# Performance work log

Measured on AMD Instinct MI355X. Metric: run time of the kernel, lower is better.

The kernel has to match this reference:

```python
import jax, jax.numpy as jnp
import numpy as np

B, N, E_PER = 64, 1024, 32768
IN_DIM, HID, K = 128, 128, 64
EPS = 1e-15


def setup_inputs() -> dict:
    key = jax.random.key(0)
    ks = jax.random.split(key, 16)
    x = jax.random.normal(ks[0], (B * N, IN_DIM), jnp.float32)
    off = (jnp.arange(B, dtype=jnp.int32) * N)[:, None]
    src = (jax.random.randint(ks[1], (B, E_PER), 0, N, dtype=jnp.int32) + off).reshape(-1)
    dst = (jax.random.randint(ks[2], (B, E_PER), 0, N, dtype=jnp.int32) + off).reshape(-1)
    edge_index = jnp.stack([src, dst])
    batch = jnp.repeat(jnp.arange(B, dtype=jnp.int32), N)

    def lin(k, i, o):
        return (jax.random.normal(k, (i, o), jnp.float32) / np.sqrt(i)).astype(jnp.float32)

    params = dict(
        W1l=lin(ks[3], IN_DIM, HID), b1l=jnp.zeros((HID,), jnp.float32), W1r=lin(ks[4], IN_DIM, HID),
        W2l=lin(ks[5], HID, K), b2l=jnp.zeros((K,), jnp.float32), W2r=lin(ks[6], HID, K),
        Wm=lin(ks[7], K, K), bm=jnp.zeros((K,), jnp.float32),
        Wrel=lin(ks[8], HID, HID), Wroot=lin(ks[9], HID, HID), broot=jnp.zeros((HID,), jnp.float32),
        Wc1=lin(ks[10], HID * K, HID), bc1=jnp.zeros((HID,), jnp.float32),
        Wc2=lin(ks[11], HID, 1), bc2=jnp.zeros((1,), jnp.float32),
    )
    return dict(x=x, edge_index=edge_index, batch=batch, num_graphs=B, nodes_per_graph=N, **params)


def _sage(x, src, dst, Wl, bl, Wr, n):
    # PyG SAGEConv: lin_l(mean_{j in N(i)} x_j) + lin_r(x_i); lin_r has no bias.
    agg = jax.ops.segment_sum(x[src], dst, num_segments=n)
    deg = jax.ops.segment_sum(jnp.ones((src.shape[0],), x.dtype), dst, num_segments=n)
    agg = agg / jnp.maximum(deg, 1.0)[:, None]
    return agg @ Wl + bl + x @ Wr


def reference(x, edge_index, batch, num_graphs, nodes_per_graph,
              W1l, b1l, W1r, W2l, b2l, W2r, Wm, bm,
              Wrel, Wroot, broot, Wc1, bc1, Wc2, bc2):
    Bn, Nn = num_graphs, nodes_per_graph
    n_total = Bn * Nn
    src, dst = edge_index[0], edge_index[1]

    z = jax.nn.leaky_relu(_sage(x, src, dst, W1l, b1l, W1r, n_total), 0.01)
    s = jax.nn.leaky_relu(_sage(z, src, dst, W2l, b2l, W2r, n_total), 0.01)
    s = s @ Wm + bm

    # to_dense_batch (equal-size graphs -> mask all True) and to_dense_adj
    z = z.reshape(Bn, Nn, -1)                      # [B, N, HID]
    s = s.reshape(Bn, Nn, -1)                      # [B, N, K]
    a = jnp.zeros((Bn, Nn, Nn), x.dtype).at[src // Nn, src % Nn, dst % Nn].add(1.0)

    # dense_diff_pool
    s = jax.nn.softmax(s, axis=-1)
    pooled = jnp.einsum('bnk,bnf->bkf', s, z)      # [B, K, HID]
    adj_p = jnp.einsum('bnk,bnm,bml->bkl', s, a, s)  # [B, K, K]
    link_loss = jnp.sqrt(jnp.sum((a - jnp.einsum('bnk,bmk->bnm', s, s)) ** 2)) / a.size
    ent_loss = jnp.mean(jnp.sum(-s * jnp.log(s + EPS), axis=-1))

    # DenseSAGEConv: lin_rel(adj@x / deg) + lin_root(x)
    agg = jnp.matmul(adj_p, pooled) / jnp.maximum(adj_p.sum(-1, keepdims=True), 1.0)
    h = jax.nn.leaky_relu(agg @ Wrel + pooled @ Wroot + broot, 0.01)

    h = h.reshape(Bn, -1)                          # [B, K*HID]
    logits = (jax.nn.leaky_relu(h @ Wc1 + bc1, 0.01) @ Wc2 + bc2).squeeze(-1)
    return logits, link_loss + ent_loss
```

## Files before the change

kernel.cpp:

```cpp
#include <hip/hip_runtime.h>
#include <math.h>

#define BATCH 64
#define NPG 1024
#define NT (BATCH*NPG)
#define EPER 32768
#define ETOT (BATCH*EPER)

typedef __attribute__((ext_vector_type(4))) float f32x4;
typedef __attribute__((ext_vector_type(8))) short s16x8;

__device__ __forceinline__ float lky(float x){ return x > 0.f ? x : 0.01f*x; }
__device__ __forceinline__ unsigned short f2bf(float f){
    unsigned u = __float_as_uint(f);
    u = u + 0x7FFFu + ((u >> 16) & 1u);
    return (unsigned short)(u >> 16);
}
__device__ __forceinline__ float bf2f_lo(unsigned v){ return __uint_as_float(v << 16); }
__device__ __forceinline__ float bf2f_hi(unsigned v){ return __uint_as_float(v & 0xFFFF0000u); }

__global__ void k_castx(const float* __restrict__ in, unsigned short* __restrict__ out, int n4){
    int i = blockIdx.x*256 + threadIdx.x;
    if (i < n4){
        float4 v = ((const float4*)in)[i];
        ushort4 o = { f2bf(v.x), f2bf(v.y), f2bf(v.z), f2bf(v.w) };
        ((ushort4*)out)[i] = o;
    }
}

__global__ void k_wprep(const float* __restrict__ W1l, const float* __restrict__ W1r,
                        const float* __restrict__ W2l, const float* __restrict__ W2r,
                        unsigned short* __restrict__ wt){
    int i = blockIdx.x*256 + threadIdx.x;
    if (i < 16384){ int k = i >> 7, n = i & 127; wt[n*128 + k] = f2bf(W1l[i]); }
    else if (i < 32768){ int j = i - 16384; int k = j >> 7, n = j & 127; wt[16384 + n*128 + k] = f2bf(W1r[j]); }
    else if (i < 40960){ int j = i - 32768; int k = j >> 6, n = j & 63; wt[32768 + n*128 + k] = f2bf(W2l[j]); }
    else if (i < 49152){ int j = i - 40960; int k = j >> 6, n = j & 63; wt[40960 + n*128 + k] = f2bf(W2r[j]); }
}

__global__ void __launch_bounds__(1024) k_a2lds(const int* __restrict__ src, const int* __restrict__ dst,
                                                unsigned* __restrict__ acc_out){
    __shared__ unsigned nib[32768];
    __shared__ unsigned red[16];
    int b = blockIdx.x, pass = blockIdx.y, tid = threadIdx.x;
    for (int i = tid; i < 32768; i += 1024) nib[i] = 0;
    __syncthreads();
    int base = b*EPER;
    for (int i = tid; i < EPER; i += 1024){
        unsigned key = (((unsigned)src[base+i] & 1023u) << 10) | ((unsigned)dst[base+i] & 1023u);
        if ((int)(key >> 18) == pass)
            atomicAdd(&nib[(key & 0x3FFFFu) >> 3], 1u << ((key & 7u)*4u));
    }
    __syncthreads();
    unsigned local = 0;
    for (int i = tid; i < 32768; i += 1024){
        unsigned w = nib[i];
        if (w){
            #pragma unroll
            for (int q = 0; q < 8; q++){ unsigned c = (w >> (4*q)) & 15u; local += c*c; }
        }
    }
    for (int o = 32; o; o >>= 1) local += __shfl_xor(local, o);
    if ((tid & 63) == 0) red[tid >> 6] = local;
    __syncthreads();
    if (tid == 0){
        unsigned s = 0;
        for (int q = 0; q < 16; q++) s += red[q];
        atomicAdd(acc_out, s);
    }
}

__global__ void __launch_bounds__(1024) k_csr(const int* __restrict__ src, const int* __restrict__ dst,
                                              int* __restrict__ ipd, int* __restrict__ ips,
                                              unsigned short* __restrict__ lst_d,
                                              unsigned short* __restrict__ lst_s){
    __shared__ unsigned eds[EPER];
    __shared__ int cnt[1024];
    __shared__ int buf[1024];
    int g = blockIdx.x, which = blockIdx.y, tid = threadIdx.x;
    cnt[tid] = 0;
    __syncthreads();
    int base = g*EPER;
    for (int i = tid; i < EPER; i += 1024){
        unsigned s = (unsigned)src[base+i] & 1023u;
        unsigned d = (unsigned)dst[base+i] & 1023u;
        eds[i] = (s << 10) | d;
        atomicAdd(&cnt[which ? s : d], 1);
    }
    __syncthreads();
    int v = cnt[tid];
    int x = v;
    buf[tid] = x; __syncthreads();
    for (int off = 1; off < 1024; off <<= 1){
        int t = (tid >= off) ? buf[tid - off] : 0;
        __syncthreads();
        x += t; buf[tid] = x; __syncthreads();
    }
    int excl = x - v;
    int* ip = which ? ips : ipd;
    ip[g*1024 + tid] = base + excl;
    if (g == 0 && tid == 0) ip[NT] = ETOT;
    cnt[tid] = excl;
    __syncthreads();
    unsigned short* lst = which ? lst_s : lst_d;
    for (int i = tid; i < EPER; i += 1024){
        unsigned key = eds[i];
        unsigned d = key & 1023u, s = key >> 10;
        unsigned idx = which ? s : d;
        unsigned val = which ? d : s;
        int p = atomicAdd(&cnt[idx], 1);
        lst[base + p] = (unsigned short)val;
    }
}

template<int MODE, int TD>
__global__ void __launch_bounds__(1024) k_aggl(
        const unsigned short* __restrict__ X, const int* __restrict__ indptr,
        const unsigned short* __restrict__ lst,
        const unsigned short* __restrict__ R, const float* __restrict__ bias,
        unsigned short* __restrict__ out){
    __shared__ uint2 tab[1024*17];
    int bid = blockIdx.x;
    int xcd = bid & 7, j = bid >> 3;
    int gi = j >> 2, part = j & 3;
    int graph = xcd + 8*gi;
    int half, nbase_loc, nchunks;
    if (TD == 128){ half = part >> 1; nbase_loc = (part & 1)*512; nchunks = 8; }
    else          { half = 0;         nbase_loc = part*256;       nchunks = 4; }
    int foff = half*64;
    int tid = threadIdx.x;
    int gb = graph*NPG;
    for (int i = tid; i < 16384; i += 1024){
        int row = i >> 4, q = i & 15;
        tab[row*17 + q] = *(const uint2*)&X[(size_t)(gb+row)*TD + foff + q*4];
    }
    __syncthreads();
    int g = tid & 15;
    for (int c = 0; c < nchunks; c++){
        int node = gb + nbase_loc + c*64 + (tid >> 4);
        int st = indptr[node], en = indptr[node+1];
        float a0 = 0.f, a1 = 0.f, a2 = 0.f, a3 = 0.f;
        int e = st;
        for (; e + 4 <= en; e += 4){
            int r0 = lst[e+0], r1 = lst[e+1], r2 = lst[e+2], r3 = lst[e+3];
            uint2 v0 = tab[r0*17 + g];
            uint2 v1 = tab[r1*17 + g];
            uint2 v2 = tab[r2*17 + g];
            uint2 v3 = tab[r3*17 + g];
            a0 += bf2f_lo(v0.x) + bf2f_lo(v1.x) + bf2f_lo(v2.x) + bf2f_lo(v3.x);
            a1 += bf2f_hi(v0.x) + bf2f_hi(v1.x) + bf2f_hi(v2.x) + bf2f_hi(v3.x);
            a2 += bf2f_lo(v0.y) + bf2f_lo(v1.y) + bf2f_lo(v2.y) + bf2f_lo(v3.y);
            a3 += bf2f_hi(v0.y) + bf2f_hi(v1.y) + bf2f_hi(v2.y) + bf2f_hi(v3.y);
        }
        for (; e < en; e++){
            uint2 v = tab[lst[e]*17 + g];
            a0 += bf2f_lo(v.x); a1 += bf2f_hi(v.x);
            a2 += bf2f_lo(v.y); a3 += bf2f_hi(v.y);
        }
        if (MODE >= 1){
            int dg = en - st;
            float inv = 1.f/(float)(dg > 1 ? dg : 1);
            a0 *= inv; a1 *= inv; a2 *= inv; a3 *= inv;
        }
        if (MODE == 2){
            uint2 r = *(const uint2*)&R[(size_t)node*TD + foff + 4*g];
            a0 = lky(a0 + bf2f_lo(r.x) + bias[foff + 4*g + 0]);
            a1 = lky(a1 + bf2f_hi(r.x) + bias[foff + 4*g + 1]);
            a2 = lky(a2 + bf2f_lo(r.y) + bias[foff + 4*g + 2]);
            a3 = lky(a3 + bf2f_hi(r.y) + bias[foff + 4*g + 3]);
        }
        uint2 pk;
        pk.x = (unsigned)f2bf(a0) | ((unsigned)f2bf(a1) << 16);
        pk.y = (unsigned)f2bf(a2) | ((unsigned)f2bf(a3) << 16);
        *(uint2*)&out[(size_t)node*TD + foff + 4*g] = pk;
    }
}

template<int N>
__global__ void __launch_bounds__(512) k_mfma2b(
        const unsigned short* __restrict__ Ah, const unsigned short* __restrict__ Wt1,
        const unsigned short* __restrict__ Wt2, unsigned short* __restrict__ C1,
        unsigned short* __restrict__ C2){
    __shared__ unsigned short ldsB[2*N*128];
    int tid = threadIdx.x;
    for (int i = tid; i < N*64; i += 512){
        int n = i >> 6, kk = i & 63;
        int swz = (n*256 + 4*kk) ^ ((n & 7) << 4);
        *(unsigned*)((char*)ldsB + swz)         = ((const unsigned*)Wt1)[i];
        *(unsigned*)((char*)ldsB + N*256 + swz) = ((const unsigned*)Wt2)[i];
    }
    __syncthreads();
    int wave = tid >> 6, l = tid & 63;
    int lr = l & 15, lg = l >> 4;
    constexpr int NF = N/16;
    int arow = blockIdx.x*128 + wave*16 + lr;
    f32x4 acc1[NF], acc2[NF];
    f32x4 zv = {0.f, 0.f, 0.f, 0.f};
    #pragma unroll
    for (int nf = 0; nf < NF; nf++){ acc1[nf] = zv; acc2[nf] = zv; }
    #pragma unroll
    for (int ks = 0; ks < 4; ks++){
        s16x8 af = *(const s16x8*)(Ah + (size_t)arow*128 + ks*32 + lg*8);
        #pragma unroll
        for (int nf = 0; nf < NF; nf++){
            int n = nf*16 + lr;
            int swz = (n*256 + ks*64 + lg*16) ^ ((n & 7) << 4);
            s16x8 b1 = *(const s16x8*)((const char*)ldsB + swz);
            s16x8 b2 = *(const s16x8*)((const char*)ldsB + N*256 + swz);
            acc1[nf] = __builtin_amdgcn_mfma_f32_16x16x32_bf16(af, b1, acc1[nf], 0, 0, 0);
            acc2[nf] = __builtin_amdgcn_mfma_f32_16x16x32_bf16(af, b2, acc2[nf], 0, 0, 0);
        }
    }
    int orow = blockIdx.x*128 + wave*16 + lg*4;
    #pragma unroll
    for (int nf = 0; nf < NF; nf++){
        int c = nf*16 + lr;
        #pragma unroll
        for (int j = 0; j < 4; j++){
            size_t idx = (size_t)(orow + j)*N + c;
            C1[idx] = f2bf(acc1[nf][j]);
            C2[idx] = f2bf(acc2[nf][j]);
        }
    }
}

__global__ void __launch_bounds__(256) k_gemm(
        const float* __restrict__ A1, const float* __restrict__ A2,
        const float* __restrict__ W1, const float* __restrict__ W2,
        const float* __restrict__ bias, void* __restrict__ C,
        int M, int Nn, int Kd, int dual, int act, int obf){
    __shared__ float sA1[16*68], sB1[16*68], sA2[16*68], sB2[16*68];
    int tid = threadIdx.x;
    int m0 = blockIdx.x*64, n0 = blockIdx.y*64;
    int tx = tid & 15, ty = tid >> 4;
    int lr = tid >> 2, lk = (tid & 3)*4;
    int wk = tid >> 4, wn = (tid & 15)*4;
    float acc[4][4] = {};
    for (int k0 = 0; k0 < Kd; k0 += 16){
        float4 a1 = *(const float4*)&A1[(size_t)(m0+lr)*Kd + k0 + lk];
        float4 w1 = *(const float4*)&W1[(size_t)(k0+wk)*Nn + n0 + wn];
        sA1[(lk+0)*68+lr] = a1.x; sA1[(lk+1)*68+lr] = a1.y;
        sA1[(lk+2)*68+lr] = a1.z; sA1[(lk+3)*68+lr] = a1.w;
        *(float4*)&sB1[wk*68+wn] = w1;
        if (dual){
            float4 a2 = *(const float4*)&A2[(size_t)(m0+lr)*Kd + k0 + lk];
            float4 w2 = *(const float4*)&W2[(size_t)(k0+wk)*Nn + n0 + wn];
            sA2[(lk+0)*68+lr] = a2.x; sA2[(lk+1)*68+lr] = a2.y;
            sA2[(lk+2)*68+lr] = a2.z; sA2[(lk+3)*68+lr] = a2.w;
            *(float4*)&sB2[wk*68+wn] = w2;
        }
        __syncthreads();
        #pragma unroll
        for (int kk = 0; kk < 16; kk++){
            float4 av = *(const float4*)&sA1[kk*68 + ty*4];
            float4 bv = *(const float4*)&sB1[kk*68 + tx*4];
            float a[4] = {av.x, av.y, av.z, av.w};
            float b[4] = {bv.x, bv.y, bv.z, bv.w};
            #pragma unroll
            for (int i = 0; i < 4; i++)
                #pragma unroll
                for (int j = 0; j < 4; j++) acc[i][j] += a[i]*b[j];
            if (dual){
                float4 av2 = *(const float4*)&sA2[kk*68 + ty*4];
                float4 bv2 = *(const float4*)&sB2[kk*68 + tx*4];
                float a2[4] = {av2.x, av2.y, av2.z, av2.w};
                float b2[4] = {bv2.x, bv2.y, bv2.z, bv2.w};
                #pragma unroll
                for (int i = 0; i < 4; i++)
                    #pragma unroll
                    for (int j = 0; j < 4; j++) acc[i][j] += a2[i]*b2[j];
            }
        }
        __syncthreads();
    }
    float bb[4] = {0.f, 0.f, 0.f, 0.f};
    if (bias){
        #pragma unroll
        for (int j = 0; j < 4; j++) bb[j] = bias[n0 + tx*4 + j];
    }
    #pragma unroll
    for (int i = 0; i < 4; i++){
        float v0 = acc[i][0]+bb[0], v1 = acc[i][1]+bb[1], v2 = acc[i][2]+bb[2], v3 = acc[i][3]+bb[3];
        if (act){ v0 = lky(v0); v1 = lky(v1); v2 = lky(v2); v3 = lky(v3); }
        size_t idx = (size_t)(m0 + ty*4 + i)*Nn + n0 + tx*4;
        if (obf){
            ushort4 o = { f2bf(v0), f2bf(v1), f2bf(v2), f2bf(v3) };
            *(ushort4*)&((unsigned short*)C)[idx] = o;
        } else {
            float4 o = { v0, v1, v2, v3 };
            *(float4*)&((float*)C)[idx] = o;
        }
    }
}

__global__ void __launch_bounds__(256) k_gemm_wm(
        const unsigned short* __restrict__ agg2h, const unsigned short* __restrict__ r2h,
        const float* __restrict__ b2l, const float* __restrict__ Wm,
        const float* __restrict__ bm,
        unsigned short* __restrict__ Sh, float* __restrict__ ent_acc){
    __shared__ float sA[16*68], sB[16*68];
    __shared__ float red[256];
    int tid = threadIdx.x;
    int m0 = blockIdx.x*64;
    int tx = tid & 15, ty = tid >> 4;
    int lr = tid >> 2, lk = (tid & 3)*4;
    int wk = tid >> 4, wn = (tid & 15)*4;
    float acc[4][4] = {};
    for (int k0 = 0; k0 < 64; k0 += 16){
        uint2 a = *(const uint2*)&agg2h[(size_t)(m0+lr)*64 + k0 + lk];
        uint2 r = *(const uint2*)&r2h[(size_t)(m0+lr)*64 + k0 + lk];
        sA[(lk+0)*68+lr] = lky(bf2f_lo(a.x) + bf2f_lo(r.x) + b2l[k0+lk+0]);
        sA[(lk+1)*68+lr] = lky(bf2f_hi(a.x) + bf2f_hi(r.x) + b2l[k0+lk+1]);
        sA[(lk+2)*68+lr] = lky(bf2f_lo(a.y) + bf2f_lo(r.y) + b2l[k0+lk+2]);
        sA[(lk+3)*68+lr] = lky(bf2f_hi(a.y) + bf2f_hi(r.y) + b2l[k0+lk+3]);
        *(float4*)&sB[wk*68+wn] = *(const float4*)&Wm[(size_t)(k0+wk)*64 + wn];
        __syncthreads();
        #pragma unroll
        for (int kk = 0; kk < 16; kk++){
            float4 av = *(const float4*)&sA[kk*68 + ty*4];
            float4 bv = *(const float4*)&sB[kk*68 + tx*4];
            float a4[4] = {av.x, av.y, av.z, av.w};
            float b4[4] = {bv.x, bv.y, bv.z, bv.w};
            #pragma unroll
            for (int i = 0; i < 4; i++)
                #pragma unroll
                for (int j = 0; j < 4; j++) acc[i][j] += a4[i]*b4[j];
        }
        __syncthreads();
    }
    float bb[4];
    #pragma unroll
    for (int j = 0; j < 4; j++) bb[j] = bm[tx*4 + j];
    float ent_local = 0.f;
    #pragma unroll
    for (int i = 0; i < 4; i++){
        float v[4];
        #pragma unroll
        for (int j = 0; j < 4; j++) v[j] = acc[i][j] + bb[j];
        float m = fmaxf(fmaxf(v[0], v[1]), fmaxf(v[2], v[3]));
        for (int o = 1; o < 16; o <<= 1) m = fmaxf(m, __shfl_xor(m, o));
        float e[4];
        float sm = 0.f;
        #pragma unroll
        for (int j = 0; j < 4; j++){ e[j] = __expf(v[j] - m); sm += e[j]; }
        for (int o = 1; o < 16; o <<= 1) sm += __shfl_xor(sm, o);
        float inv = 1.f/sm;
        float p[4];
        float w = 0.f;
        #pragma unroll
        for (int j = 0; j < 4; j++){
            p[j] = e[j]*inv;
            w += -p[j]*__logf(p[j] + 1e-15f);
        }
        for (int o = 1; o < 16; o <<= 1) w += __shfl_xor(w, o);
        if (tx == 0) ent_local += w;
        size_t idx = (size_t)(m0 + ty*4 + i)*64 + tx*4;
        ushort4 oh = { f2bf(p[0]), f2bf(p[1]), f2bf(p[2]), f2bf(p[3]) };
        *(ushort4*)&Sh[idx] = oh;
    }
    red[tid] = ent_local; __syncthreads();
    for (int o = 128; o; o >>= 1){ if (tid < o) red[tid] += red[tid+o]; __syncthreads(); }
    if (tid == 0) atomicAdd(ent_acc, red[0]);
}

__global__ void __launch_bounds__(1024) k_spmm(
        const unsigned short* __restrict__ Sh, const unsigned short* __restrict__ Zh,
        const unsigned short* __restrict__ Th,
        float* __restrict__ P, float* __restrict__ AP, float* __restrict__ GR,
        float* __restrict__ crossp, float* __restrict__ normgp){
    __shared__ unsigned short At[64*72];
    __shared__ unsigned short Bt[256*72];
    __shared__ float rtr[16], rsq[16];
    int b = blockIdx.x, tid = threadIdx.x;
    int w = tid >> 6, l = tid & 63;
    int lr = l & 15, lg = l >> 4;
    int mt = w & 3, ng = w >> 2;
    f32x4 acc[4];
    f32x4 zv = {0.f, 0.f, 0.f, 0.f};
    #pragma unroll
    for (int q = 0; q < 4; q++) acc[q] = zv;
    int gb = b*NPG;
    int sa_n = tid & 63, sa_c = (tid >> 6)*4;
    int sb_k = tid & 63, sb_g = tid >> 6;
    for (int n0 = 0; n0 < NPG; n0 += 64){
        ushort4 sv = *(const ushort4*)&Sh[(size_t)(gb+n0+sa_n)*64 + sa_c];
        At[(sa_c+0)*72 + sa_n] = sv.x;
        At[(sa_c+1)*72 + sa_n] = sv.y;
        At[(sa_c+2)*72 + sa_n] = sv.z;
        At[(sa_c+3)*72 + sa_n] = sv.w;
        {
            int R = gb + n0 + sb_k;
            const unsigned short* srcp;
            if (sb_g < 8)       srcp = &Zh[(size_t)R*128 + sb_g*16];
            else if (sb_g < 12) srcp = &Th[(size_t)R*64 + (sb_g-8)*16];
            else                srcp = &Sh[(size_t)R*64 + (sb_g-12)*16];
            ushort4 a0 = *(const ushort4*)(srcp);
            ushort4 a1 = *(const ushort4*)(srcp+4);
            ushort4 a2 = *(const ushort4*)(srcp+8);
            ushort4 a3 = *(const ushort4*)(srcp+12);
            int cb = sb_g*16;
            Bt[(cb+ 0)*72+sb_k]=a0.x; Bt[(cb+ 1)*72+sb_k]=a0.y; Bt[(cb+ 2)*72+sb_k]=a0.z; Bt[(cb+ 3)*72+sb_k]=a0.w;
            Bt[(cb+ 4)*72+sb_k]=a1.x; Bt[(cb+ 5)*72+sb_k]=a1.y; Bt[(cb+ 6)*72+sb_k]=a1.z; Bt[(cb+ 7)*72+sb_k]=a1.w;
            Bt[(cb+ 8)*72+sb_k]=a2.x; Bt[(cb+ 9)*72+sb_k]=a2.y; Bt[(cb+10)*72+sb_k]=a2.z; Bt[(cb+11)*72+sb_k]=a2.w;
            Bt[(cb+12)*72+sb_k]=a3.x; Bt[(cb+13)*72+sb_k]=a3.y; Bt[(cb+14)*72+sb_k]=a3.z; Bt[(cb+15)*72+sb_k]=a3.w;
        }
        __syncthreads();
        #pragma unroll
        for (int ks = 0; ks < 2; ks++){
            s16x8 af = *(const s16x8*)&At[(mt*16+lr)*72 + ks*32 + lg*8];
            #pragma unroll
            for (int q = 0; q < 4; q++){
                s16x8 bf = *(const s16x8*)&Bt[((ng*4+q)*16+lr)*72 + ks*32 + lg*8];
                acc[q] = __builtin_amdgcn_mfma_f32_16x16x32_bf16(af, bf, acc[q], 0, 0, 0);
            }
        }
        __syncthreads();
    }
    float tr = 0.f, sq = 0.f;
    #pragma unroll
    for (int q = 0; q < 4; q++){
        int col = (ng*4+q)*16 + lr;
        #pragma unroll
        for (int j = 0; j < 4; j++){
            int m = mt*16 + lg*4 + j;
            float v = acc[q][j];
            if (col < 128){
                P[((size_t)b*64+m)*128 + col] = v;
            } else if (col < 192){
                AP[((size_t)b*64+m)*64 + (col-128)] = v;
                if (col-128 == m) tr += v;
            } else {
                GR[((size_t)b*64+m)*64 + (col-192)] = v;
                sq += v*v;
            }
        }
    }
    for (int o = 32; o; o >>= 1){ tr += __shfl_xor(tr, o); sq += __shfl_xor(sq, o); }
    if (l == 0){ rtr[w] = tr; rsq[w] = sq; }
    __syncthreads();
    if (tid == 0){
        float str = 0.f, ssq = 0.f;
        for (int i = 0; i < 16; i++){ str += rtr[i]; ssq += rsq[i]; }
        atomicAdd(crossp, str);
        atomicAdd(normgp, ssq);
    }
}

__global__ void __launch_bounds__(256) k_heada(
        const float* __restrict__ AP, const float* __restrict__ P,
        float* __restrict__ aggout){
    __shared__ float sapT[64*65];
    __shared__ float sp[64*33];
    __shared__ float srs[64];
    int b = blockIdx.x, c0 = blockIdx.y*32;
    int tid = threadIdx.x;
    for (int i = tid; i < 4096; i += 256){
        int k = i >> 6, l = i & 63;
        sapT[l*65 + k] = AP[(size_t)b*4096 + i];
    }
    for (int i = tid; i < 2048; i += 256){
        int l = i >> 5, j = i & 31;
        sp[l*33 + j] = P[(size_t)b*8192 + l*128 + c0 + j];
    }
    __syncthreads();
    if (tid < 64){
        float s = 0.f;
        for (int l = 0; l < 64; l++) s += sapT[l*65 + tid];
        srs[tid] = fmaxf(s, 1.f);
    }
    __syncthreads();
    int k = tid & 63, jg = (tid >> 6)*8;
    float acc[8] = {};
    for (int l = 0; l < 64; l++){
        float a = sapT[l*65 + k];
        #pragma unroll
        for (int j = 0; j < 8; j++) acc[j] += a*sp[l*33 + jg + j];
    }
    float inv = 1.f/srs[k];
    #pragma unroll
    for (int j = 0; j < 8; j++)
        aggout[(size_t)b*8192 + k*128 + c0 + jg + j] = acc[j]*inv;
}

__global__ void __launch_bounds__(256) k_head2(
        const float* __restrict__ hbuf, const float* __restrict__ Wc1,
        float* __restrict__ hcacc){
    __shared__ float sh[512];
    __shared__ float sred[256];
    int b = blockIdx.x >> 4, ch = blockIdx.x & 15;
    int tid = threadIdx.x;
    for (int i = tid; i < 512; i += 256) sh[i] = hbuf[(size_t)b*8192 + ch*512 + i];
    __syncthreads();
    int j = tid & 127, half = tid >> 7;
    float acc = 0.f;
    const float* W = Wc1 + (size_t)(ch*512 + half*256)*128;
    const float* hh = sh + half*256;
    for (int r = 0; r < 256; r++) acc += hh[r]*W[(size_t)r*128 + j];
    sred[tid] = acc; __syncthreads();
    if (tid < 128) atomicAdd(&hcacc[(size_t)b*128 + tid], sred[tid] + sred[tid+128]);
}

__global__ void k_head3(const float* __restrict__ hcacc, const float* __restrict__ bc1,
                        const float* __restrict__ Wc2, const float* __restrict__ bc2,
                        float* __restrict__ out){
    int b = blockIdx.x, t = threadIdx.x;
    float hc = lky(hcacc[(size_t)b*128 + t] + bc1[t]);
    float p = hc*Wc2[t];
    for (int o = 32; o; o >>= 1) p += __shfl_xor(p, o);
    __shared__ float r2[2];
    if ((t & 63) == 0) r2[t >> 6] = p;
    __syncthreads();
    if (t == 0) out[b] = r2[0] + r2[1] + bc2[0];
}

__global__ void k_finalize(const unsigned int* __restrict__ a2,
                           const float* __restrict__ cross,
                           const float* __restrict__ normg,
                           const float* __restrict__ ent,
                           float* __restrict__ out){
    float ss = (float)(*a2) - 2.f*(*cross) + (*normg);
    if (ss < 0.f) ss = 0.f;
    float link = sqrtf(ss) / 67108864.f;
    out[64] = link + (*ent)/(float)NT;
}

extern "C" void kernel_launch(void* const* d_in, const int* in_sizes, int n_in,
                              void* d_out, int out_size, void* d_ws, size_t ws_size,
                              hipStream_t stream){
    const float* x    = (const float*)d_in[0];
    const int*   ei   = (const int*)d_in[1];
    const int*   src  = ei;
    const int*   dst  = ei + ETOT;
    const float* W1l  = (const float*)d_in[5];
    const float* b1l  = (const float*)d_in[6];
    const float* W1r  = (const float*)d_in[7];
    const float* W2l  = (const float*)d_in[8];
    const float* b2l  = (const float*)d_in[9];
    const float* W2r  = (const float*)d_in[10];
    const float* Wm   = (const float*)d_in[11];
    const float* bm   = (const float*)d_in[12];
    const float* Wrel = (const float*)d_in[13];
    const float* Wroot= (const float*)d_in[14];
    const float* broot= (const float*)d_in[15];
    const float* Wc1  = (const float*)d_in[16];
    const float* bc1  = (const float*)d_in[17];
    const float* Wc2  = (const float*)d_in[18];
    const float* bc2  = (const float*)d_in[19];
    float* out = (float*)d_out;

    char* w = (char*)d_ws;
    size_t off = 0;
    auto take = [&](size_t bytes)->void*{
        void* p = w + off; off = (off + bytes + 255) & ~(size_t)255; return p;
    };
    const size_t MB = 1024*1024;
    float* hcacc  = (float*)take((size_t)BATCH*128*4);
    float* accb   = (float*)take(64);
    size_t zero_small = off;
    unsigned short* wt = (unsigned short*)take((size_t)49152*2);
    float* pooled = (float*)take((size_t)BATCH*64*128*4);
    float* adjp   = (float*)take((size_t)BATCH*64*64*4);
    float* gram   = (float*)take((size_t)BATCH*64*64*4);
    int*   ipd   = (int*)take((size_t)(NT+1)*4);
    int*   ips   = (int*)take((size_t)(NT+1)*4);
    unsigned short* lst_d = (unsigned short*)take((size_t)ETOT*2);
    unsigned short* lst_s = (unsigned short*)take((size_t)ETOT*2);
    char*  regA  = (char*)take(16*MB);
    char*  regB  = (char*)take(16*MB);
    char*  regC  = (char*)take(16*MB);
    char*  regD  = (char*)take(16*MB);
    char*  regE  = (char*)take(16*MB);
    float* hbuf  = (float*)take((size_t)BATCH*8192*4);
    float* aggo  = (float*)take((size_t)BATCH*8192*4);

    unsigned short* y1h   = (unsigned short*)regB;
    unsigned short* th    = (unsigned short*)regB;
    unsigned short* r1h   = (unsigned short*)regC;
    unsigned short* y2h   = (unsigned short*)regC;
    unsigned short* s2h   = (unsigned short*)(regC + 8*MB);
    unsigned short* r2h   = (unsigned short*)regD;
    unsigned short* xh    = (unsigned short*)regE;
    unsigned short* zh    = (unsigned short*)regE;
    unsigned short* agg2h = (unsigned short*)regA;

    float* crossp = accb + 0;
    float* normgp = accb + 1;
    float* entp   = accb + 2;
    unsigned int* a2p = (unsigned int*)(accb + 3);

    hipMemsetAsync(d_ws, 0, zero_small, stream);

    k_wprep<<<192, 256, 0, stream>>>(W1l, W1r, W2l, W2r, wt);
    k_castx<<<NT*128/4/256, 256, 0, stream>>>(x, xh, NT*128/4);

    k_a2lds<<<dim3(BATCH, 4), 1024, 0, stream>>>(src, dst, a2p);

    k_csr<<<dim3(BATCH, 2), 1024, 0, stream>>>(src, dst, ipd, ips, lst_d, lst_s);

    k_mfma2b<128><<<NT/128, 512, 0, stream>>>(xh, wt, wt + 16384, y1h, r1h);
    k_aggl<2,128><<<256, 1024, 0, stream>>>(y1h, ipd, lst_d, r1h, b1l, zh);

    k_mfma2b<64><<<NT/128, 512, 0, stream>>>(zh, wt + 32768, wt + 40960, y2h, r2h);
    k_aggl<1,64><<<256, 1024, 0, stream>>>(y2h, ipd, lst_d, nullptr, nullptr, agg2h);
    k_gemm_wm<<<NT/64, 256, 0, stream>>>(agg2h, r2h, b2l, Wm, bm, s2h, entp);

    k_aggl<0,64><<<256, 1024, 0, stream>>>(s2h, ips, lst_s, nullptr, nullptr, th);

    k_spmm<<<BATCH, 1024, 0, stream>>>(s2h, zh, th, pooled, adjp, gram, crossp, normgp);

    k_heada<<<dim3(BATCH, 4), 256, 0, stream>>>(adjp, pooled, aggo);
    k_gemm<<<dim3(BATCH*64/64, 2), 256, 0, stream>>>(aggo, pooled, Wrel, Wroot, broot, hbuf, BATCH*64, 128, 128, 1, 1, 0);
    k_head2<<<BATCH*16, 256, 0, stream>>>(hbuf, Wc1, hcacc);
    k_head3<<<BATCH, 128, 0, stream>>>(hcacc, bc1, Wc2, bc2, out);
    k_finalize<<<1, 1, 0, stream>>>(a2p, crossp, normgp, entp, out);
}
```

Measured before the change: 306.9 us.

## Stage edge lists in LDS, drop table padding, split TD=128 aggregation over more blocks

The neighbor-aggregation kernel now copies each block's slice of the CSR neighbor list into shared memory once, then reads indices from LDS instead of global memory, with a fallback path when the slice exceeds capacity. The feature table padding (stride 17) is removed to save LDS, which may introduce bank conflicts on row gathers. For the 128-wide layer the grid doubles to 512 blocks of 256 nodes each, trading more redundant table loads for more parallelism and less per-block serial work.

```diff
diff --git a/kernel.cpp b/kernel.cpp
--- a/kernel.cpp
+++ b/kernel.cpp
@@ -6,6 +6,7 @@
 #define NT (BATCH*NPG)
 #define EPER 32768
 #define ETOT (BATCH*EPER)
+#define ECAP 10240
 
 typedef __attribute__((ext_vector_type(4))) float f32x4;
 typedef __attribute__((ext_vector_type(8))) short s16x8;
@@ -119,43 +120,59 @@
         const unsigned short* __restrict__ lst,
         const unsigned short* __restrict__ R, const float* __restrict__ bias,
         unsigned short* __restrict__ out){
-    __shared__ uint2 tab[1024*17];
+    __shared__ uint2 tab[1024*16];
+    __shared__ unsigned short elds[ECAP];
+    constexpr int PARTS = (TD == 128) ? 8 : 4;
     int bid = blockIdx.x;
     int xcd = bid & 7, j = bid >> 3;
-    int gi = j >> 2, part = j & 3;
+    int gi = j / PARTS, part = j - gi*PARTS;
     int graph = xcd + 8*gi;
-    int half, nbase_loc, nchunks;
-    if (TD == 128){ half = part >> 1; nbase_loc = (part & 1)*512; nchunks = 8; }
-    else          { half = 0;         nbase_loc = part*256;       nchunks = 4; }
+    int half = (TD == 128) ? (part >> 2) : 0;
+    int nbase_loc = (part & 3)*256;
     int foff = half*64;
     int tid = threadIdx.x;
     int gb = graph*NPG;
     for (int i = tid; i < 16384; i += 1024){
         int row = i >> 4, q = i & 15;
-        tab[row*17 + q] = *(const uint2*)&X[(size_t)(gb+row)*TD + foff + q*4];
+        tab[row*16 + q] = *(const uint2*)&X[(size_t)(gb+row)*TD + foff + q*4];
+    }
+    int estart = indptr[gb + nbase_loc];
+    int eend   = indptr[gb + nbase_loc + 256];
+    int ecount = eend - estart;
+    bool staged = (ecount <= ECAP);
+    if (staged){
+        for (int i = tid; i < ecount; i += 1024) elds[i] = lst[estart + i];
     }
     __syncthreads();
     int g = tid & 15;
-    for (int c = 0; c < nchunks; c++){
+    for (int c = 0; c < 4; c++){
         int node = gb + nbase_loc + c*64 + (tid >> 4);
         int st = indptr[node], en = indptr[node+1];
         float a0 = 0.f, a1 = 0.f, a2 = 0.f, a3 = 0.f;
-        int e = st;
-        for (; e + 4 <= en; e += 4){
-            int r0 = lst[e+0], r1 = lst[e+1], r2 = lst[e+2], r3 = lst[e+3];
-            uint2 v0 = tab[r0*17 + g];
-            uint2 v1 = tab[r1*17 + g];
-            uint2 v2 = tab[r2*17 + g];
-            uint2 v3 = tab[r3*17 + g];
-            a0 += bf2f_lo(v0.x) + bf2f_lo(v1.x) + bf2f_lo(v2.x) + bf2f_lo(v3.x);
-            a1 += bf2f_hi(v0.x) + bf2f_hi(v1.x) + bf2f_hi(v2.x) + bf2f_hi(v3.x);
-            a2 += bf2f_lo(v0.y) + bf2f_lo(v1.y) + bf2f_lo(v2.y) + bf2f_lo(v3.y);
-            a3 += bf2f_hi(v0.y) + bf2f_hi(v1.y) + bf2f_hi(v2.y) + bf2f_hi(v3.y);
-        }
-        for (; e < en; e++){
-            uint2 v = tab[lst[e]*17 + g];
-            a0 += bf2f_lo(v.x); a1 += bf2f_hi(v.x);
-            a2 += bf2f_lo(v.y); a3 += bf2f_hi(v.y);
+        if (staged){
+            int e = st - estart, ee = en - estart;
+            for (; e + 4 <= ee; e += 4){
+                int r0 = elds[e+0], r1 = elds[e+1], r2 = elds[e+2], r3 = elds[e+3];
+                uint2 v0 = tab[r0*16 + g];
+                uint2 v1 = tab[r1*16 + g];
+                uint2 v2 = tab[r2*16 + g];
+                uint2 v3 = tab[r3*16 + g];
+                a0 += bf2f_lo(v0.x) + bf2f_lo(v1.x) + bf2f_lo(v2.x) + bf2f_lo(v3.x);
+                a1 += bf2f_hi(v0.x) + bf2f_hi(v1.x) + bf2f_hi(v2.x) + bf2f_hi(v3.x);
+                a2 += bf2f_lo(v0.y) + bf2f_lo(v1.y) + bf2f_lo(v2.y) + bf2f_lo(v3.y);
+                a3 += bf2f_hi(v0.y) + bf2f_hi(v1.y) + bf2f_hi(v2.y) + bf2f_hi(v3.y);
+            }
+            for (; e < ee; e++){
+                uint2 v = tab[elds[e]*16 + g];
+                a0 += bf2f_lo(v.x); a1 += bf2f_hi(v.x);
+                a2 += bf2f_lo(v.y); a3 += bf2f_hi(v.y);
+            }
+        } else {
+            for (int e = st; e < en; e++){
+                uint2 v = tab[lst[e]*16 + g];
+                a0 += bf2f_lo(v.x); a1 += bf2f_hi(v.x);
+                a2 += bf2f_lo(v.y); a3 += bf2f_hi(v.y);
+            }
         }
         if (MODE >= 1){
             int dg = en - st;
@@ -598,7 +615,7 @@
     k_csr<<<dim3(BATCH, 2), 1024, 0, stream>>>(src, dst, ipd, ips, lst_d, lst_s);
 
     k_mfma2b<128><<<NT/128, 512, 0, stream>>>(xh, wt, wt + 16384, y1h, r1h);
-    k_aggl<2,128><<<256, 1024, 0, stream>>>(y1h, ipd, lst_d, r1h, b1l, zh);
+    k_aggl<2,128><<<512, 1024, 0, stream>>>(y1h, ipd, lst_d, r1h, b1l, zh);
 
     k_mfma2b<64><<<NT/128, 512, 0, stream>>>(zh, wt + 32768, wt + 40960, y2h, r2h);
     k_aggl<1,64><<<256, 1024, 0, stream>>>(y2h, ipd, lst_d, nullptr, nullptr, agg2h);
```

New measurement: 315.6 us. 1.03x slower.
